# Kernel optimization log

Hardware: AMD Instinct MI355X
Metric: run time of the kernel (lower is better)

The kernel has to match this reference:

```python
import jax, jax.numpy as jnp
import numpy as np

DK = 64
DROPOUT_P = 0.1


def setup_inputs() -> dict:
    key = jax.random.key(0)
    kq, kk, kv, km = jax.random.split(key, 4)
    B, S, D = 16, 2048, 64
    q = jax.random.normal(kq, (B, S, D), dtype=jnp.float32)
    k = jax.random.normal(kk, (B, S, D), dtype=jnp.float32)
    v = jax.random.normal(kv, (B, S, D), dtype=jnp.float32)
    attn_mask = jax.random.randint(km, (S, S), 0, 2, dtype=jnp.int32)
    return {"q": q, "k": k, "v": v, "attn_mask": attn_mask}


def reference(q, k, v, attn_mask):
    # q = q / sqrt(dk)
    qs = q * (1.0 / np.sqrt(DK)).astype(np.float32)
    # dots: [B, S_q, S_k]
    dots = jnp.einsum("bqd,bkd->bqk", qs, k)
    # mask: 0 -> -inf, 1 -> 0 (additive)
    add_mask = jnp.where(attn_mask == 0, -jnp.inf, 0.0).astype(dots.dtype)
    dots = dots + add_mask  # broadcast [S,S] over batch
    attn = jax.nn.softmax(dots, axis=-1)
    # inverted dropout, train mode, fixed key for determinism
    keep = jax.random.bernoulli(jax.random.key(42), 1.0 - DROPOUT_P, attn.shape)
    attn = jnp.where(keep, attn * (1.0 / (1.0 - DROPOUT_P)), 0.0)
    out = jnp.einsum("bqk,bkd->bqd", attn, v)
    return out
```

## Files before the change

kernel.cpp:

```cpp
#include <hip/hip_runtime.h>

#define BATCH 16
#define SEQ   2048
#define DIM   64
#define NTHREADS 256

typedef short bf16x8 __attribute__((ext_vector_type(8)));
typedef float f32x4 __attribute__((ext_vector_type(4)));

__device__ __forceinline__ int ldsoff(int row) {
  return row * 72 + 16 * (row >> 2);
}
#define LDS_SZ (64 * 72 + 16 * 16)

__device__ __forceinline__ unsigned tf_bits(unsigned f) {
  unsigned x0 = 0u;
  unsigned x1 = f;
  const unsigned ks1 = 42u;
  const unsigned ks2 = 0x1BD11BDAu ^ 42u;
  x1 += ks1;
#define TF_R(r) { x0 += x1; x1 = __builtin_amdgcn_alignbit(x1, x1, 32u - (r)); x1 ^= x0; }
  TF_R(13) TF_R(15) TF_R(26) TF_R(6)
  x0 += ks1; x1 += ks2 + 1u;
  TF_R(17) TF_R(29) TF_R(16) TF_R(24)
  x0 += ks2; x1 += 2u;
  TF_R(13) TF_R(15) TF_R(26) TF_R(6)
  x1 += ks1 + 3u;
  TF_R(17) TF_R(29) TF_R(16) TF_R(24)
  x0 += ks1; x1 += ks2 + 4u;
  TF_R(13) TF_R(15) TF_R(26) TF_R(6)
  x0 += ks2; x1 += 5u;
#undef TF_R
  return x0 ^ x1;
}
#define KEEP_THRESH 0xE6666600u

__device__ __forceinline__ unsigned pack_bf16x2(float lo, float hi) {
  const unsigned l = (__float_as_uint(lo) + 0x8000u) >> 16;
  const unsigned h = (__float_as_uint(hi) + 0x8000u) & 0xFFFF0000u;
  return h | l;
}
__device__ __forceinline__ unsigned pack_trunc(float lo, float hi) {
  return __builtin_amdgcn_perm(__float_as_uint(hi), __float_as_uint(lo), 0x07060302u);
}

#define WS_KF   0
#define WS_VF   1048576
#define WS_MB   2097152
#define WS_KEEP 2228224
#define WS_O0   2883584
#define WS_O1   4980736
#define WS_L    7077888

#define KEEPRNG_BLKS 5120
#define MASK_BLKS    1024
#define CONV_BLKS    2048

__global__ __launch_bounds__(NTHREADS, 8)
void prep(const float* __restrict__ k, const float* __restrict__ v,
          const int* __restrict__ mask, unsigned* __restrict__ ws) {
  const int t = threadIdx.x;
  const unsigned bx = blockIdx.x;

  if (bx < KEEPRNG_BLKS) {
    const unsigned pid = bx * NTHREADS + (unsigned)t;
    const unsigned R4 = pid / 160u;
    const unsigned c  = pid - R4 * 160u;
    const unsigned base = R4 * 8192u + c * 4u + 1408u;
    unsigned k16 = 0u;
#pragma unroll
    for (int r = 0; r < 4; ++r)
#pragma unroll
      for (int cc = 0; cc < 4; ++cc)
        k16 |= (tf_bits(base + (unsigned)(r * 2048 + cc)) < KEEP_THRESH)
                   ? (1u << (r * 4 + cc)) : 0u;
    ((unsigned short*)(ws + WS_KEEP))[pid] = (unsigned short)k16;
    return;
  }

  if (bx < KEEPRNG_BLKS + MASK_BLKS) {
    const unsigned pid = (bx - KEEPRNG_BLKS) * NTHREADS + (unsigned)t;
    const unsigned C4 = pid & 511u, R4 = pid >> 9;
    unsigned m16 = 0u;
#pragma unroll
    for (int r = 0; r < 4; ++r) {
      const int4 mv = *(const int4*)(mask + (size_t)(4 * R4 + r) * SEQ + 4 * C4);
      m16 |= (mv.x ? 1u : 0u) << (r * 4 + 0);
      m16 |= (mv.y ? 1u : 0u) << (r * 4 + 1);
      m16 |= (mv.z ? 1u : 0u) << (r * 4 + 2);
      m16 |= (mv.w ? 1u : 0u) << (r * 4 + 3);
    }
    ((unsigned short*)(ws + WS_MB))[pid] = (unsigned short)m16;
    return;
  }

  const int lane = t & 63;
  const int tx = lane & 15, quad = lane >> 4;
  const unsigned gid = (bx - KEEPRNG_BLKS - MASK_BLKS) * NTHREADS + (unsigned)t;
  const unsigned e = gid & 262143u;
  const int ks = (e >> 6) & 1, nt = (e >> 7) & 3, kt = (e >> 9) & 31, b = e >> 14;
  uint4 wout;
  if (gid < 262144u) {
    const float* src = k + ((size_t)b * SEQ + kt * 64 + 4 * tx + nt) * DIM
                         + ks * 32 + quad * 8;
    const float4 f0 = *(const float4*)src;
    const float4 f1 = *(const float4*)(src + 4);
    wout.x = pack_bf16x2(f0.x, f0.y); wout.y = pack_bf16x2(f0.z, f0.w);
    wout.z = pack_bf16x2(f1.x, f1.y); wout.w = pack_bf16x2(f1.z, f1.w);
    *(uint4*)(ws + WS_KF + (size_t)e * 4) = wout;
  } else {
    const float* src = v + ((size_t)b * SEQ + kt * 64 + ks * 32 + quad * 8) * DIM
                         + nt * 16 + tx;
    const float a0 = src[0 * DIM], a1 = src[1 * DIM], a2 = src[2 * DIM], a3 = src[3 * DIM];
    const float a4 = src[4 * DIM], a5 = src[5 * DIM], a6 = src[6 * DIM], a7 = src[7 * DIM];
    wout.x = pack_bf16x2(a0, a1); wout.y = pack_bf16x2(a2, a3);
    wout.z = pack_bf16x2(a4, a5); wout.w = pack_bf16x2(a6, a7);
    *(uint4*)(ws + WS_VF + (size_t)e * 4) = wout;
  }
}

__global__ __launch_bounds__(NTHREADS, 6)
void attn_fwd(const float* __restrict__ q, const unsigned* __restrict__ ws,
              float* __restrict__ out) {
  __shared__ unsigned short PS[LDS_SZ];

  const int t    = threadIdx.x;
  const int w    = t >> 6;
  const int lane = t & 63;
  const int tx   = lane & 15;
  const int quad = lane >> 4;

  const int sk = (int)(blockIdx.x >> 9);
  const int r  = blockIdx.x & 511;
  const int bb = r >> 5;
  const int q0 = (r & 31) * 64;
  const int qw = q0 + 16 * w;
  const int kt0 = sk * 11;
  const int ktn = (sk == 2) ? 10 : 11;

  const float qscale = 0.125f * 1.44269504088896340736f;

  bf16x8 aq[2];
  {
    const float* qr = q + ((size_t)bb * SEQ + qw + tx) * DIM + quad * 8;
#pragma unroll
    for (int ks = 0; ks < 2; ++ks) {
      const float4 f0 = *(const float4*)(qr + ks * 32);
      const float4 f1 = *(const float4*)(qr + ks * 32 + 4);
      union { unsigned u[4]; bf16x8 v; } a;
      a.u[0] = pack_bf16x2(f0.x * qscale, f0.y * qscale);
      a.u[1] = pack_bf16x2(f0.z * qscale, f0.w * qscale);
      a.u[2] = pack_bf16x2(f1.x * qscale, f1.y * qscale);
      a.u[3] = pack_bf16x2(f1.z * qscale, f1.w * qscale);
      aq[ks] = a.v;
    }
  }

  float lrun[4] = {0.f, 0.f, 0.f, 0.f};
  f32x4 oacc[4];
#pragma unroll
  for (int nt = 0; nt < 4; ++nt) oacc[nt] = (f32x4){0.f, 0.f, 0.f, 0.f};

  const unsigned* kfb = ws + WS_KF + (size_t)(bb * 32) * 2048 + (size_t)lane * 4;
  const unsigned* vfb = ws + WS_VF + (size_t)(bb * 32) * 2048 + (size_t)lane * 4;
  const unsigned short* maskp = (const unsigned short*)(ws + WS_MB)
      + ((size_t)((qw >> 2) + quad)) * 512 + tx;
  const unsigned short* keepp = (const unsigned short*)(ws + WS_KEEP)
      + ((size_t)(bb * 512 + (qw >> 2) + quad)) * 160 + tx;
  const unsigned fbase0 = (unsigned)(bb * SEQ + qw + quad * 4) * (unsigned)SEQ
                          + (unsigned)(4 * tx);

  bf16x8 vf[4][2];

#define RNG_PWRITE(kt_, qk_, mw_)                                              \
  {                                                                            \
    const unsigned fb = fbase0 + (unsigned)((kt_) * 64);                       \
    _Pragma("unroll")                                                          \
    for (int reg = 0; reg < 4; ++reg) {                                        \
      const unsigned mnib = (mw_) >> (reg * 4);                                \
      float pd[4];                                                             \
      float ls = 0.0f;                                                         \
      _Pragma("unroll")                                                        \
      for (int nt = 0; nt < 4; ++nt) {                                         \
        const float s = (mnib & (1u << nt)) ? qk_[nt][reg] : -1e30f;           \
        const float e = __builtin_amdgcn_exp2f(s);                             \
        ls += e;                                                               \
        const unsigned bits = tf_bits(fb + (unsigned)(reg * SEQ) + (unsigned)nt); \
        pd[nt] = (bits < KEEP_THRESH) ? e : 0.0f;                              \
      }                                                                        \
      lrun[reg] += ls;                                                         \
      uint2 pw;                                                                \
      pw.x = pack_trunc(pd[0], pd[1]);                                         \
      pw.y = pack_trunc(pd[2], pd[3]);                                         \
      *(uint2*)&PS[ldsoff(16 * w + quad * 4 + reg) + 4 * tx] = pw;             \
    }                                                                          \
  }

#define PATCH_PWRITE(qk_, kw_, mw_)                                            \
  {                                                                            \
    const unsigned cwd = (kw_) & (mw_);                                        \
    _Pragma("unroll")                                                          \
    for (int reg = 0; reg < 4; ++reg) {                                        \
      const unsigned mnib = (mw_) >> (reg * 4);                                \
      const unsigned cnib = cwd >> (reg * 4);                                  \
      float pd[4];                                                             \
      float ls = 0.0f;                                                         \
      _Pragma("unroll")                                                        \
      for (int nt = 0; nt < 4; ++nt) {                                         \
        const float s = (mnib & (1u << nt)) ? qk_[nt][reg] : -1e30f;           \
        const float e = __builtin_amdgcn_exp2f(s);                             \
        ls += e;                                                               \
        pd[nt] = (cnib & (1u << nt)) ? e : 0.0f;                               \
      }                                                                        \
      lrun[reg] += ls;                                                         \
      uint2 pw;                                                                \
      pw.x = pack_trunc(pd[0], pd[1]);                                         \
      pw.y = pack_trunc(pd[2], pd[3]);                                         \
      *(uint2*)&PS[ldsoff(16 * w + quad * 4 + reg) + 4 * tx] = pw;             \
    }                                                                          \
  }

#define LOAD_KF(kt_)                                                           \
    const unsigned* kfp = kfb + (size_t)(kt_) * 2048;                          \
    bf16x8 kf[4][2];                                                           \
    _Pragma("unroll")                                                          \
    for (int nt = 0; nt < 4; ++nt)                                             \
      _Pragma("unroll")                                                        \
      for (int ks = 0; ks < 2; ++ks)                                           \
        kf[nt][ks] = *(const bf16x8*)(kfp + (nt * 2 + ks) * 256);

#define PV_STEP                                                                \
    _Pragma("unroll")                                                          \
    for (int ks = 0; ks < 2; ++ks) {                                           \
      const bf16x8 ap = *(const bf16x8*)&PS[ldsoff(16 * w + tx) + ks * 32 + quad * 8]; \
      _Pragma("unroll")                                                        \
      for (int nt = 0; nt < 4; ++nt)                                           \
        oacc[nt] = __builtin_amdgcn_mfma_f32_16x16x32_bf16(ap, vf[nt][ks],     \
                                                           oacc[nt], 0, 0, 0); \
    }

#define LOAD_VF(kt_)                                                           \
    const unsigned* vfp = vfb + (size_t)(kt_) * 2048;                          \
    _Pragma("unroll")                                                          \
    for (int nt = 0; nt < 4; ++nt)                                             \
      _Pragma("unroll")                                                        \
      for (int ks = 0; ks < 2; ++ks)                                           \
        vf[nt][ks] = *(const bf16x8*)(vfp + (nt * 2 + ks) * 256);

#define QK_STEP(qk_)                                                           \
    f32x4 qk_[4];                                                              \
    _Pragma("unroll")                                                          \
    for (int nt = 0; nt < 4; ++nt) {                                           \
      f32x4 c = (f32x4){0.f, 0.f, 0.f, 0.f};                                   \
      _Pragma("unroll")                                                        \
      for (int ks = 0; ks < 2; ++ks)                                           \
        c = __builtin_amdgcn_mfma_f32_16x16x32_bf16(aq[ks], kf[nt][ks], c, 0, 0, 0); \
      qk_[nt] = c;                                                             \
    }

  if (sk != 2) {
    {
      LOAD_KF(kt0)
      LOAD_VF(kt0)
      const unsigned mwv = maskp[kt0 * 16];
      QK_STEP(qk)
      RNG_PWRITE(kt0, qk, mwv)
    }
#pragma unroll 1
    for (int kt = kt0 + 1; kt < kt0 + 11; ++kt) {
      LOAD_KF(kt)
      const unsigned mwv = maskp[kt * 16];
      PV_STEP
      LOAD_VF(kt)
      QK_STEP(qk)
      RNG_PWRITE(kt, qk, mwv)
    }
  } else {
    {
      LOAD_KF(22)
      LOAD_VF(22)
      const unsigned kwv = keepp[0];
      const unsigned mwv = maskp[22 * 16];
      QK_STEP(qk)
      PATCH_PWRITE(qk, kwv, mwv)
    }
#pragma unroll 1
    for (int kt = 23; kt < 32; ++kt) {
      LOAD_KF(kt)
      const unsigned kwv = keepp[(kt - 22) * 16];
      const unsigned mwv = maskp[kt * 16];
      PV_STEP
      LOAD_VF(kt)
      QK_STEP(qk)
      PATCH_PWRITE(qk, kwv, mwv)
    }
  }

  PV_STEP

  float lsum[4];
#pragma unroll
  for (int reg = 0; reg < 4; ++reg) {
    float ls = lrun[reg];
    ls += __shfl_xor(ls, 1);
    ls += __shfl_xor(ls, 2);
    ls += __shfl_xor(ls, 4);
    ls += __shfl_xor(ls, 8);
    lsum[reg] = ls;
  }
  float* wsf = (float*)ws;
  const size_t off = ((size_t)bb * SEQ + qw) * DIM;
  float* ob = (sk == 0) ? wsf + WS_O0 + off
            : (sk == 1) ? wsf + WS_O1 + off
                        : out + off;
#pragma unroll
  for (int nt = 0; nt < 4; ++nt)
#pragma unroll
    for (int reg = 0; reg < 4; ++reg)
      ob[(size_t)(quad * 4 + reg) * DIM + nt * 16 + tx] = oacc[nt][reg];
  if (tx == 0) {
    float* lp = wsf + WS_L + sk * 32768 + bb * SEQ + qw + quad * 4;
#pragma unroll
    for (int reg = 0; reg < 4; ++reg) lp[reg] = lsum[reg];
  }
}

__global__ __launch_bounds__(NTHREADS)
void combine(float* __restrict__ out, const unsigned* __restrict__ ws) {
  const unsigned gid = blockIdx.x * NTHREADS + threadIdx.x;
  const float* wsf = (const float*)ws;
  const float4 a  = ((const float4*)out)[gid];
  const float4 b0 = ((const float4*)(wsf + WS_O0))[gid];
  const float4 b1 = ((const float4*)(wsf + WS_O1))[gid];
  const unsigned row = gid >> 4;
  const float linv = (1.0f / 0.9f) / (wsf[WS_L + row] + wsf[WS_L + 32768u + row]
                                      + wsf[WS_L + 65536u + row]);
  float4 o;
  o.x = (a.x + b0.x + b1.x) * linv;
  o.y = (a.y + b0.y + b1.y) * linv;
  o.z = (a.z + b0.z + b1.z) * linv;
  o.w = (a.w + b0.w + b1.w) * linv;
  ((float4*)out)[gid] = o;
}

extern "C" void kernel_launch(void* const* d_in, const int* in_sizes, int n_in,
                              void* d_out, int out_size, void* d_ws, size_t ws_size,
                              hipStream_t stream) {
  const float* q = (const float*)d_in[0];
  const float* k = (const float*)d_in[1];
  const float* v = (const float*)d_in[2];
  const int* mask = (const int*)d_in[3];
  float* out = (float*)d_out;
  unsigned* ws = (unsigned*)d_ws;

  hipLaunchKernelGGL(prep, dim3(KEEPRNG_BLKS + MASK_BLKS + CONV_BLKS),
                     dim3(NTHREADS), 0, stream, k, v, mask, ws);
  hipLaunchKernelGGL(attn_fwd, dim3(1536), dim3(NTHREADS), 0, stream,
                     q, ws, out);
  hipLaunchKernelGGL(combine, dim3(2048), dim3(NTHREADS), 0, stream, out, ws);
}
```

Before: 242.3 us.

## Drop precomputed keep-bit prep stage; compute dropout RNG inline for all splits

```diff
diff --git a/kernel.cpp b/kernel.cpp
--- a/kernel.cpp
+++ b/kernel.cpp
@@ -44,79 +44,63 @@
   return __builtin_amdgcn_perm(__float_as_uint(hi), __float_as_uint(lo), 0x07060302u);
 }
 
-#define WS_KF   0
-#define WS_VF   1048576
-#define WS_MB   2097152
-#define WS_KEEP 2228224
-#define WS_O0   2883584
-#define WS_O1   4980736
-#define WS_L    7077888
-
-#define KEEPRNG_BLKS 5120
-#define MASK_BLKS    1024
-#define CONV_BLKS    2048
-
-__global__ __launch_bounds__(NTHREADS, 8)
+#define WS_KF 0
+#define WS_VF 1048576
+#define WS_MB 2097152
+#define WS_O0 2228224
+#define WS_O1 4325376
+#define WS_L  6422528
+
+__global__ __launch_bounds__(NTHREADS)
 void prep(const float* __restrict__ k, const float* __restrict__ v,
           const int* __restrict__ mask, unsigned* __restrict__ ws) {
   const int t = threadIdx.x;
   const unsigned bx = blockIdx.x;
 
-  if (bx < KEEPRNG_BLKS) {
-    const unsigned pid = bx * NTHREADS + (unsigned)t;
-    const unsigned R4 = pid / 160u;
-    const unsigned c  = pid - R4 * 160u;
-    const unsigned base = R4 * 8192u + c * 4u + 1408u;
-    unsigned k16 = 0u;
-#pragma unroll
-    for (int r = 0; r < 4; ++r)
-#pragma unroll
-      for (int cc = 0; cc < 4; ++cc)
-        k16 |= (tf_bits(base + (unsigned)(r * 2048 + cc)) < KEEP_THRESH)
-                   ? (1u << (r * 4 + cc)) : 0u;
-    ((unsigned short*)(ws + WS_KEEP))[pid] = (unsigned short)k16;
+  if (bx < 2048) {
+    const int x = (int)bx & 7;
+    const int j = (int)bx >> 3;
+    const int b = 2 * x + (j & 1);
+    const int inner = j >> 1;
+    const int kv = inner >> 6;
+    const int idx = inner & 63;
+    const unsigned e = (unsigned)b * 16384u + (unsigned)idx * 256u + (unsigned)t;
+    const int lane = t & 63;
+    const int tx = lane & 15, quad = lane >> 4;
+    const int ks = (e >> 6) & 1, nt = (e >> 7) & 3, kt = (e >> 9) & 31;
+    uint4 wout;
+    if (kv == 0) {
+      const float* src = k + ((size_t)b * SEQ + kt * 64 + 4 * tx + nt) * DIM
+                           + ks * 32 + quad * 8;
+      const float4 f0 = *(const float4*)src;
+      const float4 f1 = *(const float4*)(src + 4);
+      wout.x = pack_bf16x2(f0.x, f0.y); wout.y = pack_bf16x2(f0.z, f0.w);
+      wout.z = pack_bf16x2(f1.x, f1.y); wout.w = pack_bf16x2(f1.z, f1.w);
+      *(uint4*)(ws + WS_KF + (size_t)e * 4) = wout;
+    } else {
+      const float* src = v + ((size_t)b * SEQ + kt * 64 + ks * 32 + quad * 8) * DIM
+                           + nt * 16 + tx;
+      const float a0 = src[0 * DIM], a1 = src[1 * DIM], a2 = src[2 * DIM], a3 = src[3 * DIM];
+      const float a4 = src[4 * DIM], a5 = src[5 * DIM], a6 = src[6 * DIM], a7 = src[7 * DIM];
+      wout.x = pack_bf16x2(a0, a1); wout.y = pack_bf16x2(a2, a3);
+      wout.z = pack_bf16x2(a4, a5); wout.w = pack_bf16x2(a6, a7);
+      *(uint4*)(ws + WS_VF + (size_t)e * 4) = wout;
+    }
     return;
   }
 
-  if (bx < KEEPRNG_BLKS + MASK_BLKS) {
-    const unsigned pid = (bx - KEEPRNG_BLKS) * NTHREADS + (unsigned)t;
-    const unsigned C4 = pid & 511u, R4 = pid >> 9;
-    unsigned m16 = 0u;
-#pragma unroll
-    for (int r = 0; r < 4; ++r) {
-      const int4 mv = *(const int4*)(mask + (size_t)(4 * R4 + r) * SEQ + 4 * C4);
-      m16 |= (mv.x ? 1u : 0u) << (r * 4 + 0);
-      m16 |= (mv.y ? 1u : 0u) << (r * 4 + 1);
-      m16 |= (mv.z ? 1u : 0u) << (r * 4 + 2);
-      m16 |= (mv.w ? 1u : 0u) << (r * 4 + 3);
-    }
-    ((unsigned short*)(ws + WS_MB))[pid] = (unsigned short)m16;
-    return;
-  }
-
-  const int lane = t & 63;
-  const int tx = lane & 15, quad = lane >> 4;
-  const unsigned gid = (bx - KEEPRNG_BLKS - MASK_BLKS) * NTHREADS + (unsigned)t;
-  const unsigned e = gid & 262143u;
-  const int ks = (e >> 6) & 1, nt = (e >> 7) & 3, kt = (e >> 9) & 31, b = e >> 14;
-  uint4 wout;
-  if (gid < 262144u) {
-    const float* src = k + ((size_t)b * SEQ + kt * 64 + 4 * tx + nt) * DIM
-                         + ks * 32 + quad * 8;
-    const float4 f0 = *(const float4*)src;
-    const float4 f1 = *(const float4*)(src + 4);
-    wout.x = pack_bf16x2(f0.x, f0.y); wout.y = pack_bf16x2(f0.z, f0.w);
-    wout.z = pack_bf16x2(f1.x, f1.y); wout.w = pack_bf16x2(f1.z, f1.w);
-    *(uint4*)(ws + WS_KF + (size_t)e * 4) = wout;
-  } else {
-    const float* src = v + ((size_t)b * SEQ + kt * 64 + ks * 32 + quad * 8) * DIM
-                         + nt * 16 + tx;
-    const float a0 = src[0 * DIM], a1 = src[1 * DIM], a2 = src[2 * DIM], a3 = src[3 * DIM];
-    const float a4 = src[4 * DIM], a5 = src[5 * DIM], a6 = src[6 * DIM], a7 = src[7 * DIM];
-    wout.x = pack_bf16x2(a0, a1); wout.y = pack_bf16x2(a2, a3);
-    wout.z = pack_bf16x2(a4, a5); wout.w = pack_bf16x2(a6, a7);
-    *(uint4*)(ws + WS_VF + (size_t)e * 4) = wout;
-  }
+  const unsigned pid = (bx - 2048u) * NTHREADS + (unsigned)t;
+  const unsigned C4 = pid & 511u, R4 = pid >> 9;
+  unsigned m16 = 0u;
+#pragma unroll
+  for (int rr = 0; rr < 4; ++rr) {
+    const int4 mv = *(const int4*)(mask + (size_t)(4 * R4 + rr) * SEQ + 4 * C4);
+    m16 |= (mv.x ? 1u : 0u) << (rr * 4 + 0);
+    m16 |= (mv.y ? 1u : 0u) << (rr * 4 + 1);
+    m16 |= (mv.z ? 1u : 0u) << (rr * 4 + 2);
+    m16 |= (mv.w ? 1u : 0u) << (rr * 4 + 3);
+  }
+  ((unsigned short*)(ws + WS_MB))[pid] = (unsigned short)m16;
 }
 
 __global__ __launch_bounds__(NTHREADS, 6)
@@ -130,13 +114,15 @@
   const int tx   = lane & 15;
   const int quad = lane >> 4;
 
-  const int sk = (int)(blockIdx.x >> 9);
-  const int r  = blockIdx.x & 511;
-  const int bb = r >> 5;
-  const int q0 = (r & 31) * 64;
+  const int x  = (int)blockIdx.x & 7;
+  const int j  = (int)blockIdx.x >> 3;
+  const int bb = 2 * x + (j & 1);
+  const int j2 = j >> 1;
+  const int q0 = (j2 & 31) * 64;
+  const int sk = j2 >> 5;
   const int qw = q0 + 16 * w;
   const int kt0 = sk * 11;
-  const int ktn = (sk == 2) ? 10 : 11;
+  const int ktend = (sk == 2) ? 32 : kt0 + 11;
 
   const float qscale = 0.125f * 1.44269504088896340736f;
 
@@ -165,8 +151,6 @@
   const unsigned* vfb = ws + WS_VF + (size_t)(bb * 32) * 2048 + (size_t)lane * 4;
   const unsigned short* maskp = (const unsigned short*)(ws + WS_MB)
       + ((size_t)((qw >> 2) + quad)) * 512 + tx;
-  const unsigned short* keepp = (const unsigned short*)(ws + WS_KEEP)
-      + ((size_t)(bb * 512 + (qw >> 2) + quad)) * 160 + tx;
   const unsigned fbase0 = (unsigned)(bb * SEQ + qw + quad * 4) * (unsigned)SEQ
                           + (unsigned)(4 * tx);
 
@@ -196,30 +180,6 @@
     }                                                                          \
   }
 
-#define PATCH_PWRITE(qk_, kw_, mw_)                                            \
-  {                                                                            \
-    const unsigned cwd = (kw_) & (mw_);                                        \
-    _Pragma("unroll")                                                          \
-    for (int reg = 0; reg < 4; ++reg) {                                        \
-      const unsigned mnib = (mw_) >> (reg * 4);                                \
-      const unsigned cnib = cwd >> (reg * 4);                                  \
-      float pd[4];                                                             \
-      float ls = 0.0f;                                                         \
-      _Pragma("unroll")                                                        \
-      for (int nt = 0; nt < 4; ++nt) {                                         \
-        const float s = (mnib & (1u << nt)) ? qk_[nt][reg] : -1e30f;           \
-        const float e = __builtin_amdgcn_exp2f(s);                             \
-        ls += e;                                                               \
-        pd[nt] = (cnib & (1u << nt)) ? e : 0.0f;                               \
-      }                                                                        \
-      lrun[reg] += ls;                                                         \
-      uint2 pw;                                                                \
-      pw.x = pack_trunc(pd[0], pd[1]);                                         \
-      pw.y = pack_trunc(pd[2], pd[3]);                                         \
-      *(uint2*)&PS[ldsoff(16 * w + quad * 4 + reg) + 4 * tx] = pw;             \
-    }                                                                          \
-  }
-
 #define LOAD_KF(kt_)                                                           \
     const unsigned* kfp = kfb + (size_t)(kt_) * 2048;                          \
     bf16x8 kf[4][2];                                                           \
@@ -258,44 +218,22 @@
       qk_[nt] = c;                                                             \
     }
 
-  if (sk != 2) {
-    {
-      LOAD_KF(kt0)
-      LOAD_VF(kt0)
-      const unsigned mwv = maskp[kt0 * 16];
-      QK_STEP(qk)
-      RNG_PWRITE(kt0, qk, mwv)
-    }
+  {
+    LOAD_KF(kt0)
+    LOAD_VF(kt0)
+    const unsigned mwv = maskp[kt0 * 16];
+    QK_STEP(qk)
+    RNG_PWRITE(kt0, qk, mwv)
+  }
 #pragma unroll 1
-    for (int kt = kt0 + 1; kt < kt0 + 11; ++kt) {
-      LOAD_KF(kt)
-      const unsigned mwv = maskp[kt * 16];
-      PV_STEP
-      LOAD_VF(kt)
-      QK_STEP(qk)
-      RNG_PWRITE(kt, qk, mwv)
-    }
-  } else {
-    {
-      LOAD_KF(22)
-      LOAD_VF(22)
-      const unsigned kwv = keepp[0];
-      const unsigned mwv = maskp[22 * 16];
-      QK_STEP(qk)
-      PATCH_PWRITE(qk, kwv, mwv)
-    }
-#pragma unroll 1
-    for (int kt = 23; kt < 32; ++kt) {
-      LOAD_KF(kt)
-      const unsigned kwv = keepp[(kt - 22) * 16];
-      const unsigned mwv = maskp[kt * 16];
-      PV_STEP
-      LOAD_VF(kt)
-      QK_STEP(qk)
-      PATCH_PWRITE(qk, kwv, mwv)
-    }
-  }
-
+  for (int kt = kt0 + 1; kt < ktend; ++kt) {
+    LOAD_KF(kt)
+    const unsigned mwv = maskp[kt * 16];
+    PV_STEP
+    LOAD_VF(kt)
+    QK_STEP(qk)
+    RNG_PWRITE(kt, qk, mwv)
+  }
   PV_STEP
 
   float lsum[4];
@@ -353,8 +291,8 @@
   float* out = (float*)d_out;
   unsigned* ws = (unsigned*)d_ws;
 
-  hipLaunchKernelGGL(prep, dim3(KEEPRNG_BLKS + MASK_BLKS + CONV_BLKS),
-                     dim3(NTHREADS), 0, stream, k, v, mask, ws);
+  hipLaunchKernelGGL(prep, dim3(3072), dim3(NTHREADS), 0, stream,
+                     k, v, mask, ws);
   hipLaunchKernelGGL(attn_fwd, dim3(1536), dim3(NTHREADS), 0, stream,
                      q, ws, out);
   hipLaunchKernelGGL(combine, dim3(2048), dim3(NTHREADS), 0, stream, out, ws);
```

After: 232.9 us. 1.04x faster.
